# Optimization experiments

Hardware: AMD Instinct MI355X
Metric: run time of the kernel (lower is better)

## Reference

```python
import jax, jax.numpy as jnp
import numpy as np
import math

B, L, D = 2, 2048, 2048
H, DH = 16, 128
R = 16
WIN = 512
EPS = 1e-6


def setup_inputs() -> dict:
    key = jax.random.key(0)
    ks = jax.random.split(key, 16)
    def rn(k, shape, s=1.0):
        return jax.random.normal(k, shape, dtype=jnp.float32) * s
    d_in_std = 1.0 / math.sqrt(D)
    return {
        "x": rn(ks[0], (B, L, D)),
        "norm_w": jnp.ones((D,), jnp.float32),
        "wq": rn(ks[1], (H * DH, D), d_in_std),
        "wk": rn(ks[2], (H * DH, D), d_in_std),
        "wv": rn(ks[3], (H * DH, D), d_in_std),
        "wo": rn(ks[4], (D, H * DH), d_in_std),
        "qA": rn(ks[5], (R, D), 0.02), "qB": rn(ks[6], (H * DH, R), 0.02),
        "kA": rn(ks[7], (R, D), 0.02), "kB": rn(ks[8], (H * DH, R), 0.02),
        "vA": rn(ks[9], (R, D), 0.02), "vB": rn(ks[10], (H * DH, R), 0.02),
        "oA": rn(ks[11], (R, H * DH), 0.02), "oB": rn(ks[12], (D, R), 0.02),
    }


def _lora_proj(h, Wb, A, Bm, scale):
    # y = h @ Wb^T + ((h @ A^T) @ Bm^T) * scale
    return h @ Wb.T + (h @ A.T) @ Bm.T * scale


def _rope_freqs(seq_len, d_head):
    half = d_head // 2
    theta = 1.0 / (10000.0 ** (jnp.arange(half, dtype=jnp.float32) / half))
    freqs = jnp.arange(seq_len, dtype=jnp.float32)[:, None] * theta[None, :]  # (L, half)
    emb = jnp.concatenate([freqs, freqs], axis=-1)  # (L, d_head)
    return jnp.cos(emb), jnp.sin(emb)


def _apply_rope(x, cos, sin):
    # x: (B, H, L, d_head); cos/sin: (L, d_head)
    half = x.shape[-1] // 2
    x1, x2 = x[..., :half], x[..., half:]
    rotated = jnp.concatenate([-x2, x1], axis=-1)
    return x * cos[None, None] + rotated * sin[None, None]


def reference(x, norm_w, wq, wk, wv, wo, qA, qB, kA, kB, vA, vB, oA, oB):
    lora_scale = 1.0 / qA.shape[0]
    residual = x
    # RMSNorm
    h = x * jax.lax.rsqrt(jnp.mean(x * x, axis=-1, keepdims=True) + EPS) * norm_w
    # LoRA-fused projections
    Q = _lora_proj(h, wq, qA, qB, lora_scale)
    K = _lora_proj(h, wk, kA, kB, lora_scale)
    V = _lora_proj(h, wv, vA, vB, lora_scale)
    b, l, _ = x.shape
    Q = Q.reshape(b, l, H, DH).transpose(0, 2, 1, 3)
    K = K.reshape(b, l, H, DH).transpose(0, 2, 1, 3)
    V = V.reshape(b, l, H, DH).transpose(0, 2, 1, 3)
    cos, sin = _rope_freqs(l, DH)
    Q = _apply_rope(Q, cos, sin)
    K = _apply_rope(K, cos, sin)
    # sliding-window causal additive mask (L, L)
    i = jnp.arange(l)[:, None]
    j = jnp.arange(l)[None, :]
    valid = (j <= i) & (j >= i - WIN + 1)
    mask = jnp.where(valid, 0.0, -jnp.inf).astype(x.dtype)
    scores = jnp.einsum("bhqd,bhkd->bhqk", Q, K) / math.sqrt(DH)
    attn = jax.nn.softmax(scores + mask[None, None], axis=-1)
    out = jnp.einsum("bhqk,bhkd->bhqd", attn, V)
    out = out.transpose(0, 2, 1, 3).reshape(b, l, H * DH)
    out = _lora_proj(out, wo, oA, oB, lora_scale)
    return residual + out
```

## Files before the change

### kernel.cpp

```cpp
#include <hip/hip_runtime.h>
#include <hip/hip_bf16.h>

#define LNUM 2048
#define DNUM 2048
#define HNUM 16
#define DHNUM 128
#define MTOK 4096
#define WINSZ 512

typedef __attribute__((ext_vector_type(8))) short bf16x8;
typedef __attribute__((ext_vector_type(4))) short bf16x4;
typedef __attribute__((ext_vector_type(4))) float f32x4;

#define GLOBAL_AS __attribute__((address_space(1)))
#define LDS_AS __attribute__((address_space(3)))
#define BARX asm volatile("s_barrier" ::: "memory")

__device__ __forceinline__ unsigned short f2bf(float f) {
  union { float f; unsigned u; } v; v.f = f;
  unsigned r = v.u + 0x7FFFu + ((v.u >> 16) & 1u);
  return (unsigned short)(r >> 16);
}
__device__ __forceinline__ float bf2f(unsigned short h) {
  union { unsigned u; float f; } v; v.u = ((unsigned)h) << 16;
  return v.f;
}

__global__ __launch_bounds__(256) void weff_k(
    const float* __restrict__ w0, const float* __restrict__ w1,
    const float* __restrict__ w2, const float* __restrict__ w3,
    const float* __restrict__ b0, const float* __restrict__ b1,
    const float* __restrict__ b2, const float* __restrict__ b3,
    const float* __restrict__ a0, const float* __restrict__ a1,
    const float* __restrict__ a2, const float* __restrict__ a3,
    unsigned short* __restrict__ o0, unsigned short* __restrict__ o1,
    unsigned short* __restrict__ o2, unsigned short* __restrict__ o3,
    float s) {
  const int z = blockIdx.z;
  const float* W = z==0?w0:z==1?w1:z==2?w2:w3;
  const float* Bm = z==0?b0:z==1?b1:z==2?b2:b3;
  const float* Am = z==0?a0:z==1?a1:z==2?a2:a3;
  unsigned short* out = z==0?o0:z==1?o1:z==2?o2:o3;

  const int col = blockIdx.x * 1024 + threadIdx.x * 4;
  const int row0 = blockIdx.y * 64;

  float4 av[16];
  #pragma unroll
  for (int j = 0; j < 16; j++) av[j] = *(const float4*)(Am + (size_t)j * DNUM + col);

  for (int r = 0; r < 64; r++) {
    const int n = row0 + r;
    const float* brow = Bm + (size_t)n * 16;
    float dx = 0.f, dy = 0.f, dz = 0.f, dw = 0.f;
    #pragma unroll
    for (int j = 0; j < 16; j++) {
      const float bj = brow[j];
      dx = fmaf(bj, av[j].x, dx); dy = fmaf(bj, av[j].y, dy);
      dz = fmaf(bj, av[j].z, dz); dw = fmaf(bj, av[j].w, dw);
    }
    const float4 wv = *(const float4*)(W + (size_t)n * DNUM + col);
    ushort4 o;
    o.x = f2bf(wv.x + s*dx); o.y = f2bf(wv.y + s*dy);
    o.z = f2bf(wv.z + s*dz); o.w = f2bf(wv.w + s*dw);
    *(ushort4*)(out + (size_t)n * DNUM + col) = o;
  }
}

__global__ __launch_bounds__(256) void rmsnorm_k(const float* __restrict__ x,
                                                 const float* __restrict__ w,
                                                 unsigned short* __restrict__ h) {
  const int row = blockIdx.x;
  const int t = threadIdx.x;
  const float4* xr = (const float4*)(x + (size_t)row * DNUM);
  float4 v0 = xr[t];
  float4 v1 = xr[t + 256];
  float ss = v0.x*v0.x + v0.y*v0.y + v0.z*v0.z + v0.w*v0.w +
             v1.x*v1.x + v1.y*v1.y + v1.z*v1.z + v1.w*v1.w;
  #pragma unroll
  for (int off = 32; off > 0; off >>= 1) ss += __shfl_xor(ss, off);
  __shared__ float red[4];
  if ((t & 63) == 0) red[t >> 6] = ss;
  __syncthreads();
  const float r = rsqrtf((red[0]+red[1]+red[2]+red[3]) * (1.0f/DNUM) + 1e-6f);
  const float4* wr4 = (const float4*)w;
  float4 w0 = wr4[t], w1 = wr4[t+256];
  ushort4 o0, o1;
  o0.x = f2bf(v0.x*r*w0.x); o0.y = f2bf(v0.y*r*w0.y);
  o0.z = f2bf(v0.z*r*w0.z); o0.w = f2bf(v0.w*r*w0.w);
  o1.x = f2bf(v1.x*r*w1.x); o1.y = f2bf(v1.y*r*w1.y);
  o1.z = f2bf(v1.z*r*w1.z); o1.w = f2bf(v1.w*r*w1.w);
  ushort4* hp = (ushort4*)(h + (size_t)row * DNUM);
  hp[t] = o0; hp[t + 256] = o1;
}

__global__ __launch_bounds__(512, 1) void gemmqkv_k(
    const unsigned short* __restrict__ Am,
    const unsigned short* __restrict__ Wall,
    unsigned short* __restrict__ Oall)
{
  const int row0 = blockIdx.y * 256;
  const int col0 = blockIdx.x * 192;
  const int tid = threadIdx.x;
  const int wv = tid >> 6, lane = tid & 63;
  const int wr = wv >> 2, wc = wv & 3;
  const int g = lane >> 4, r4 = lane & 15;

  __shared__ unsigned short lds[57344];

  const int rp = lane >> 2;
  const int sg8 = ((lane & 3) ^ ((rp >> 1) & 3)) * 8;

  auto stage = [&](int buf, int k0) {
    #pragma unroll
    for (int q = 0; q < 4; q++) {
      const int c = q*8 + wv;
      const int kh = c & 1, rc = c >> 1;
      const unsigned short* ga = Am + (size_t)(row0 + rc*16 + rp) * DNUM + k0 + kh*32 + sg8;
      __builtin_amdgcn_global_load_lds((const GLOBAL_AS void*)ga,
          (LDS_AS void*)&lds[buf*16384 + (kh*16 + rc)*512], 16, 0, 0);
    }
    #pragma unroll
    for (int q = 0; q < 3; q++) {
      const int c = q*8 + wv;
      const int kh = c & 1, rc = c >> 1;
      const unsigned short* gb = Wall + (size_t)(col0 + rc*16 + rp) * DNUM + k0 + kh*32 + sg8;
      __builtin_amdgcn_global_load_lds((const GLOBAL_AS void*)gb,
          (LDS_AS void*)&lds[32768 + buf*12288 + (kh*12 + rc)*512], 16, 0, 0);
    }
  };

  f32x4 acc[8][3];
  #pragma unroll
  for (int m = 0; m < 8; m++)
    #pragma unroll
    for (int n = 0; n < 3; n++) acc[m][n] = f32x4{0.f,0.f,0.f,0.f};

  const int cg = (g ^ ((r4 >> 1) & 3)) * 8;

  auto compute = [&](int buf) {
    #pragma unroll
    for (int kh = 0; kh < 2; kh++) {
      const unsigned short* As = &lds[buf*16384 + kh*8192];
      const unsigned short* Bs = &lds[32768 + buf*12288 + kh*6144];
      bf16x8 af[8], bb[3];
      #pragma unroll
      for (int m = 0; m < 8; m++)
        af[m] = *(const bf16x8*)&As[(wr*8 + m)*512 + r4*32 + cg];
      #pragma unroll
      for (int n = 0; n < 3; n++)
        bb[n] = *(const bf16x8*)&Bs[(wc*3 + n)*512 + r4*32 + cg];
      #pragma unroll
      for (int m = 0; m < 8; m++)
        #pragma unroll
        for (int n = 0; n < 3; n++)
          acc[m][n] = __builtin_amdgcn_mfma_f32_16x16x32_bf16(af[m], bb[n], acc[m][n], 0, 0, 0);
    }
  };

  stage(0, 0);
  const int nt = DNUM / 64;
  for (int t = 0; t < nt; t++) {
    if (t < nt - 1) {
      stage((t + 1) & 1, (t + 1) * 64);
      asm volatile("s_waitcnt vmcnt(7)" ::: "memory");
    } else {
      asm volatile("s_waitcnt vmcnt(0)" ::: "memory");
    }
    BARX;
    compute(t & 1);
    BARX;
  }

  #pragma unroll
  for (int m = 0; m < 8; m++) {
    #pragma unroll
    for (int rg = 0; rg < 4; rg++) {
      const int row = row0 + wr*128 + m*16 + 4*g + rg;
      #pragma unroll
      for (int n = 0; n < 3; n++) {
        const int colg = col0 + wc*48 + n*16 + r4;
        const int z = colg >> 11, c = colg & 2047;
        Oall[((size_t)z * MTOK + row) * DNUM + c] = f2bf(acc[m][n][rg]);
      }
    }
  }
}

__global__ __launch_bounds__(512, 1) void gemmo_k(
    const unsigned short* __restrict__ Am,
    const unsigned short* __restrict__ W,
    const float* __restrict__ resid, float* __restrict__ Of)
{
  const int row0 = blockIdx.y * 256;
  const int col0 = blockIdx.x * 128;
  const int tid = threadIdx.x;
  const int wv = tid >> 6, lane = tid & 63;
  const int wr = wv >> 2, wc = wv & 3;
  const int g = lane >> 4, r4 = lane & 15;

  __shared__ unsigned short lds[49152];

  const int rp = lane >> 2;
  const int sg8 = ((lane & 3) ^ ((rp >> 1) & 3)) * 8;

  auto stage = [&](int buf, int k0) {
    #pragma unroll
    for (int q = 0; q < 4; q++) {
      const int c = q*8 + wv;
      const int kh = c & 1, rc = c >> 1;
      const unsigned short* ga = Am + (size_t)(row0 + rc*16 + rp) * DNUM + k0 + kh*32 + sg8;
      __builtin_amdgcn_global_load_lds((const GLOBAL_AS void*)ga,
          (LDS_AS void*)&lds[buf*16384 + (kh*16 + rc)*512], 16, 0, 0);
    }
    #pragma unroll
    for (int q = 0; q < 2; q++) {
      const int c = q*8 + wv;
      const int kh = c & 1, rc = c >> 1;
      const unsigned short* gb = W + (size_t)(col0 + rc*16 + rp) * DNUM + k0 + kh*32 + sg8;
      __builtin_amdgcn_global_load_lds((const GLOBAL_AS void*)gb,
          (LDS_AS void*)&lds[32768 + buf*8192 + (kh*8 + rc)*512], 16, 0, 0);
    }
  };

  f32x4 acc[8][2];
  #pragma unroll
  for (int m = 0; m < 8; m++)
    #pragma unroll
    for (int n = 0; n < 2; n++) acc[m][n] = f32x4{0.f,0.f,0.f,0.f};

  const int cg = (g ^ ((r4 >> 1) & 3)) * 8;

  auto compute = [&](int buf) {
    #pragma unroll
    for (int kh = 0; kh < 2; kh++) {
      const unsigned short* As = &lds[buf*16384 + kh*8192];
      const unsigned short* Bs = &lds[32768 + buf*8192 + kh*4096];
      bf16x8 af[8], bb[2];
      #pragma unroll
      for (int m = 0; m < 8; m++)
        af[m] = *(const bf16x8*)&As[(wr*8 + m)*512 + r4*32 + cg];
      #pragma unroll
      for (int n = 0; n < 2; n++)
        bb[n] = *(const bf16x8*)&Bs[(wc*2 + n)*512 + r4*32 + cg];
      #pragma unroll
      for (int m = 0; m < 8; m++)
        #pragma unroll
        for (int n = 0; n < 2; n++)
          acc[m][n] = __builtin_amdgcn_mfma_f32_16x16x32_bf16(af[m], bb[n], acc[m][n], 0, 0, 0);
    }
  };

  stage(0, 0);
  const int nt = DNUM / 64;
  for (int t = 0; t < nt; t++) {
    if (t < nt - 1) {
      stage((t + 1) & 1, (t + 1) * 64);
      asm volatile("s_waitcnt vmcnt(6)" ::: "memory");
    } else {
      asm volatile("s_waitcnt vmcnt(0)" ::: "memory");
    }
    BARX;
    compute(t & 1);
    BARX;
  }

  #pragma unroll
  for (int m = 0; m < 8; m++) {
    #pragma unroll
    for (int rg = 0; rg < 4; rg++) {
      const int row = row0 + wr*128 + m*16 + 4*g + rg;
      #pragma unroll
      for (int n = 0; n < 2; n++) {
        const int col = col0 + wc*32 + n*16 + r4;
        Of[(size_t)row * DNUM + col] = acc[m][n][rg] + resid[(size_t)row * DNUM + col];
      }
    }
  }
}

__global__ __launch_bounds__(256) void rope_k(unsigned short* __restrict__ Qm,
                                              unsigned short* __restrict__ Km) {
  const int u = blockIdx.x * 256 + threadIdx.x;
  const int t2 = u & 31;
  const int hh = (u >> 5) & (HNUM-1);
  const int i = u >> 9;
  const int l = i & (LNUM - 1);
  const int d0 = 2 * t2;
  const float C = 0.14391156831212787f;
  const float th0 = __expf(-(float)d0 * C);
  const float th1 = __expf(-(float)(d0+1) * C);
  float sn0, cs0, sn1, cs1;
  __sincosf((float)l * th0, &sn0, &cs0);
  __sincosf((float)l * th1, &sn1, &cs1);
  const size_t base = (size_t)i * DNUM + hh * DHNUM + d0;
  const float qs = 0.08838834764831845f;

  unsigned qa = *(const unsigned*)(Qm + base);
  unsigned qb = *(const unsigned*)(Qm + base + 64);
  float a0 = bf2f((unsigned short)qa), a1 = bf2f((unsigned short)(qa >> 16));
  float b0 = bf2f((unsigned short)qb), b1 = bf2f((unsigned short)(qb >> 16));
  unsigned lo = (unsigned)f2bf((a0*cs0 - b0*sn0) * qs) | ((unsigned)f2bf((a1*cs1 - b1*sn1) * qs) << 16);
  unsigned hi = (unsigned)f2bf((b0*cs0 + a0*sn0) * qs) | ((unsigned)f2bf((b1*cs1 + a1*sn1) * qs) << 16);
  *(unsigned*)(Qm + base) = lo;
  *(unsigned*)(Qm + base + 64) = hi;

  unsigned ka = *(const unsigned*)(Km + base);
  unsigned kb = *(const unsigned*)(Km + base + 64);
  a0 = bf2f((unsigned short)ka); a1 = bf2f((unsigned short)(ka >> 16));
  b0 = bf2f((unsigned short)kb); b1 = bf2f((unsigned short)(kb >> 16));
  lo = (unsigned)f2bf(a0*cs0 - b0*sn0) | ((unsigned)f2bf(a1*cs1 - b1*sn1) << 16);
  hi = (unsigned)f2bf(b0*cs0 + a0*sn0) | ((unsigned)f2bf(b1*cs1 + a1*sn1) << 16);
  *(unsigned*)(Km + base) = lo;
  *(unsigned*)(Km + base + 64) = hi;
}

__global__ __launch_bounds__(256) void attn_k(const unsigned short* __restrict__ Q,
                                              const unsigned short* __restrict__ K,
                                              const unsigned short* __restrict__ V,
                                              unsigned short* __restrict__ O) {
  __shared__ unsigned short Kls[8192];
  __shared__ unsigned short Vt[8704];
  const int tid = threadIdx.x, wv = tid >> 6, lane = tid & 63;
  const int g = lane >> 4, r4 = lane & 15;
  const int bidx = blockIdx.x;
  const int q4 = bidx & 31, hh = (bidx >> 5) & 15, b = bidx >> 9;
  const int q_base = q4 * 64;
  const int q0 = q_base + wv * 16;
  const size_t bh = (size_t)b * LNUM * DNUM + (size_t)hh * DHNUM;

  bf16x8 qf[4];
  {
    const unsigned short* qr = Q + bh + (size_t)(q0 + r4) * DNUM;
    #pragma unroll
    for (int dc = 0; dc < 4; dc++) qf[dc] = *(const bf16x8*)(qr + dc*32 + g*8);
  }
  f32x4 oacc[8];
  #pragma unroll
  for (int c = 0; c < 8; c++) oacc[c] = f32x4{0.f,0.f,0.f,0.f};
  float mrun = -1e30f, lrun = 0.f;

  const int qi = q0 + r4;
  const int lo_key = (q_base >= WINSZ) ? (q_base - WINSZ + 1) : 0;
  const int t_lo = lo_key >> 6, t_hi = q_base >> 6;

  const int rp = lane >> 2;
  const int sg = (((lane & 3) ^ ((rp >> 1) & 3))) * 8;
  const int cgr = (g ^ ((r4 >> 1) & 3)) * 8;

  const int vc = wv*8 + (lane >> 3);
  const int vd = lane & 7;

  for (int t64 = t_lo; t64 <= t_hi; t64++) {
    const int k64 = t64 * 64;
    __syncthreads();
    #pragma unroll
    for (int q = 0; q < 4; q++) {
      const unsigned short* src = K + bh + (size_t)(k64 + wv*16 + rp) * DNUM + q*32 + sg;
      __builtin_amdgcn_global_load_lds((const GLOBAL_AS void*)src,
          (LDS_AS void*)&Kls[(q*4 + wv)*512], 16, 0, 0);
    }
    #pragma unroll
    for (int p = 0; p < 2; p++) {
      const int d0 = (vd + 8*p) * 8;
      const unsigned short* vp = V + bh + (size_t)(k64 + 2*vc) * DNUM + d0;
      uint4 va = *(const uint4*)vp;
      uint4 vb = *(const uint4*)(vp + DNUM);
      const unsigned short* as = (const unsigned short*)&va;
      const unsigned short* bs = (const unsigned short*)&vb;
      #pragma unroll
      for (int j = 0; j < 8; j++) {
        *(unsigned*)&Vt[(d0 + j)*68 + 2*vc] = (unsigned)as[j] | ((unsigned)bs[j] << 16);
      }
    }
    __syncthreads();

    #pragma unroll
    for (int kts = 0; kts < 4; kts++) {
      const int k0s = k64 + kts*16;
      if (k0s > q0 + 15 || k0s + 15 < q0 - (WINSZ - 1)) continue;
      f32x4 st = f32x4{0.f,0.f,0.f,0.f};
      #pragma unroll
      for (int dc = 0; dc < 4; dc++) {
        const bf16x8 kf = *(const bf16x8*)&Kls[(dc*4 + kts)*512 + r4*32 + cgr];
        st = __builtin_amdgcn_mfma_f32_16x16x32_bf16(kf, qf[dc], st, 0, 0, 0);
      }
      const int kj = k0s + 4*g;
      const float sv0 = (kj   <= qi && kj   > qi - WINSZ) ? st[0] : -1e30f;
      const float sv1 = (kj+1 <= qi && kj+1 > qi - WINSZ) ? st[1] : -1e30f;
      const float sv2 = (kj+2 <= qi && kj+2 > qi - WINSZ) ? st[2] : -1e30f;
      const float sv3 = (kj+3 <= qi && kj+3 > qi - WINSZ) ? st[3] : -1e30f;
      float pmax = fmaxf(fmaxf(sv0, sv1), fmaxf(sv2, sv3));
      pmax = fmaxf(pmax, __shfl_xor(pmax, 16));
      pmax = fmaxf(pmax, __shfl_xor(pmax, 32));
      const float mnew = fmaxf(mrun, pmax);
      const float sc_old = __expf(mrun - mnew);
      const float p0 = __expf(sv0 - mnew), p1 = __expf(sv1 - mnew);
      const float p2 = __expf(sv2 - mnew), p3 = __expf(sv3 - mnew);
      float psum = p0 + p1 + p2 + p3;
      psum += __shfl_xor(psum, 16);
      psum += __shfl_xor(psum, 32);
      lrun = lrun * sc_old + psum;
      mrun = mnew;
      bf16x4 pf;
      pf[0] = (short)f2bf(p0); pf[1] = (short)f2bf(p1);
      pf[2] = (short)f2bf(p2); pf[3] = (short)f2bf(p3);
      #pragma unroll
      for (int c = 0; c < 8; c++) {
        oacc[c][0] *= sc_old; oacc[c][1] *= sc_old;
        oacc[c][2] *= sc_old; oacc[c][3] *= sc_old;
      }
      #pragma unroll
      for (int dblk = 0; dblk < 8; dblk++) {
        const bf16x4 vf = *(const bf16x4*)&Vt[(dblk*16 + r4)*68 + kts*16 + 4*g];
        oacc[dblk] = __builtin_amdgcn_mfma_f32_16x16x16bf16_1k(vf, pf, oacc[dblk], 0, 0, 0);
      }
    }
  }

  __syncthreads();
  unsigned short* scr = &Vt[wv * 2176];
  const float inv = 1.0f / lrun;
  #pragma unroll
  for (int dblk = 0; dblk < 8; dblk++) {
    #pragma unroll
    for (int rg = 0; rg < 4; rg++) {
      scr[r4*136 + dblk*16 + 4*g + rg] = f2bf(oacc[dblk][rg] * inv);
    }
  }
  #pragma unroll
  for (int p = 0; p < 4; p++) {
    const int qq = p*4 + g;
    const uint4 vvv = *(const uint4*)(scr + qq*136 + r4*8);
    *(uint4*)(O + bh + (size_t)(q0 + qq) * DNUM + r4*8) = vvv;
  }
}

extern "C" void kernel_launch(void* const* d_in, const int* in_sizes, int n_in,
                              void* d_out, int out_size, void* d_ws, size_t ws_size,
                              hipStream_t stream) {
  (void)in_sizes; (void)n_in; (void)out_size; (void)ws_size;
  const float* x     = (const float*)d_in[0];
  const float* normw = (const float*)d_in[1];
  const float* wq = (const float*)d_in[2];
  const float* wk = (const float*)d_in[3];
  const float* wvm = (const float*)d_in[4];
  const float* wo = (const float*)d_in[5];
  const float* qA = (const float*)d_in[6];
  const float* qB = (const float*)d_in[7];
  const float* kA = (const float*)d_in[8];
  const float* kB = (const float*)d_in[9];
  const float* vA = (const float*)d_in[10];
  const float* vB = (const float*)d_in[11];
  const float* oA = (const float*)d_in[12];
  const float* oB = (const float*)d_in[13];

  char* w = (char*)d_ws;
  const size_t SZ = (size_t)MTOK * DNUM * 2;
  unsigned short* h  = (unsigned short*)(w);
  unsigned short* Qb = (unsigned short*)(w + SZ);
  unsigned short* Kb = (unsigned short*)(w + 2*SZ);
  unsigned short* Vb = (unsigned short*)(w + 3*SZ);
  unsigned short* AO = (unsigned short*)(w + 4*SZ);
  unsigned short* Wq = (unsigned short*)(w + 5*SZ);
  unsigned short* Wk = Wq + (size_t)DNUM*DNUM;
  unsigned short* Wv = Wk + (size_t)DNUM*DNUM;
  unsigned short* Wo = Wv + (size_t)DNUM*DNUM;

  const float lscale = 1.0f / 16.0f;

  weff_k<<<dim3(2, 32, 4), 256, 0, stream>>>(wq, wk, wvm, wo,
                                             qB, kB, vB, oB,
                                             qA, kA, vA, oA,
                                             Wq, Wk, Wv, Wo, lscale);
  rmsnorm_k<<<dim3(4096), 256, 0, stream>>>(x, normw, h);
  gemmqkv_k<<<dim3(32, 16), 512, 0, stream>>>(h, Wq, Qb);
  rope_k<<<dim3(8192), 256, 0, stream>>>(Qb, Kb);
  attn_k<<<dim3(1024), 256, 0, stream>>>(Qb, Kb, Vb, AO);
  gemmo_k<<<dim3(16, 16), 512, 0, stream>>>(AO, Wo, x, (float*)d_out);
}
```

Measured before the change: 260.2 us.

## Enlarge attention tiles to 128 queries, add lazy softmax rescale and interior-mask fast path

The attention kernel now runs 8 waves per block over 128 queries, so each K/V tile loaded into LDS is shared by twice as many query rows. K and V loading is split across the 8 waves. Masking is skipped for interior tiles that lie fully inside the window. The online softmax only rescales the accumulators when the running max grows by more than a threshold, which removes most exp and multiply work but lets unnormalized values grow up to about e^8. The weight-merge kernel also uses more blocks with fewer rows each to raise parallelism.

```diff
diff --git a/kernel.cpp b/kernel.cpp
--- a/kernel.cpp
+++ b/kernel.cpp
@@ -43,13 +43,13 @@
   unsigned short* out = z==0?o0:z==1?o1:z==2?o2:o3;
 
   const int col = blockIdx.x * 1024 + threadIdx.x * 4;
-  const int row0 = blockIdx.y * 64;
+  const int row0 = blockIdx.y * 16;
 
   float4 av[16];
   #pragma unroll
   for (int j = 0; j < 16; j++) av[j] = *(const float4*)(Am + (size_t)j * DNUM + col);
 
-  for (int r = 0; r < 64; r++) {
+  for (int r = 0; r < 16; r++) {
     const int n = row0 + r;
     const float* brow = Bm + (size_t)n * 16;
     float dx = 0.f, dy = 0.f, dz = 0.f, dw = 0.f;
@@ -315,17 +315,18 @@
   *(unsigned*)(Km + base + 64) = hi;
 }
 
-__global__ __launch_bounds__(256) void attn_k(const unsigned short* __restrict__ Q,
+__global__ __launch_bounds__(512) void attn_k(const unsigned short* __restrict__ Q,
                                               const unsigned short* __restrict__ K,
                                               const unsigned short* __restrict__ V,
                                               unsigned short* __restrict__ O) {
-  __shared__ unsigned short Kls[8192];
-  __shared__ unsigned short Vt[8704];
+  __shared__ unsigned short shm[17408];
+  unsigned short* Kls = shm;
+  unsigned short* Vt  = shm + 8192;
   const int tid = threadIdx.x, wv = tid >> 6, lane = tid & 63;
   const int g = lane >> 4, r4 = lane & 15;
   const int bidx = blockIdx.x;
-  const int q4 = bidx & 31, hh = (bidx >> 5) & 15, b = bidx >> 9;
-  const int q_base = q4 * 64;
+  const int q7 = bidx & 15, hh = (bidx >> 4) & 15, b = bidx >> 8;
+  const int q_base = q7 * 128;
   const int q0 = q_base + wv * 16;
   const size_t bh = (size_t)b * LNUM * DNUM + (size_t)hh * DHNUM;
 
@@ -341,28 +342,29 @@
   float mrun = -1e30f, lrun = 0.f;
 
   const int qi = q0 + r4;
-  const int lo_key = (q_base >= WINSZ) ? (q_base - WINSZ + 1) : 0;
-  const int t_lo = lo_key >> 6, t_hi = q_base >> 6;
+  const int t_lo = (q_base >= WINSZ) ? ((q_base - WINSZ + 1) >> 6) : 0;
+  const int t_hi = (q_base + 127) >> 6;
 
   const int rp = lane >> 2;
   const int sg = (((lane & 3) ^ ((rp >> 1) & 3))) * 8;
   const int cgr = (g ^ ((r4 >> 1) & 3)) * 8;
 
-  const int vc = wv*8 + (lane >> 3);
-  const int vd = lane & 7;
+  const int vc = tid & 31;
+  const int vd = tid >> 5;
 
   for (int t64 = t_lo; t64 <= t_hi; t64++) {
     const int k64 = t64 * 64;
     __syncthreads();
     #pragma unroll
-    for (int q = 0; q < 4; q++) {
-      const unsigned short* src = K + bh + (size_t)(k64 + wv*16 + rp) * DNUM + q*32 + sg;
+    for (int qq = 0; qq < 2; qq++) {
+      const int c = wv*2 + qq;
+      const int dc = c >> 2, kc = c & 3;
+      const unsigned short* src = K + bh + (size_t)(k64 + kc*16 + rp) * DNUM + dc*32 + sg;
       __builtin_amdgcn_global_load_lds((const GLOBAL_AS void*)src,
-          (LDS_AS void*)&Kls[(q*4 + wv)*512], 16, 0, 0);
-    }
-    #pragma unroll
-    for (int p = 0; p < 2; p++) {
-      const int d0 = (vd + 8*p) * 8;
+          (LDS_AS void*)&Kls[(dc*4 + kc)*512], 16, 0, 0);
+    }
+    {
+      const int d0 = vd * 8;
       const unsigned short* vp = V + bh + (size_t)(k64 + 2*vc) * DNUM + d0;
       uint4 va = *(const uint4*)vp;
       uint4 vb = *(const uint4*)(vp + DNUM);
@@ -385,32 +387,44 @@
         const bf16x8 kf = *(const bf16x8*)&Kls[(dc*4 + kts)*512 + r4*32 + cgr];
         st = __builtin_amdgcn_mfma_f32_16x16x32_bf16(kf, qf[dc], st, 0, 0, 0);
       }
-      const int kj = k0s + 4*g;
-      const float sv0 = (kj   <= qi && kj   > qi - WINSZ) ? st[0] : -1e30f;
-      const float sv1 = (kj+1 <= qi && kj+1 > qi - WINSZ) ? st[1] : -1e30f;
-      const float sv2 = (kj+2 <= qi && kj+2 > qi - WINSZ) ? st[2] : -1e30f;
-      const float sv3 = (kj+3 <= qi && kj+3 > qi - WINSZ) ? st[3] : -1e30f;
+      float sv0, sv1, sv2, sv3;
+      const bool interior = (k0s + 15 <= q0) && (k0s >= q0 - (WINSZ - 16));
+      if (interior) {
+        sv0 = st[0]; sv1 = st[1]; sv2 = st[2]; sv3 = st[3];
+      } else {
+        const int kj = k0s + 4*g;
+        sv0 = (kj   <= qi && kj   > qi - WINSZ) ? st[0] : -INFINITY;
+        sv1 = (kj+1 <= qi && kj+1 > qi - WINSZ) ? st[1] : -INFINITY;
+        sv2 = (kj+2 <= qi && kj+2 > qi - WINSZ) ? st[2] : -INFINITY;
+        sv3 = (kj+3 <= qi && kj+3 > qi - WINSZ) ? st[3] : -INFINITY;
+      }
       float pmax = fmaxf(fmaxf(sv0, sv1), fmaxf(sv2, sv3));
       pmax = fmaxf(pmax, __shfl_xor(pmax, 16));
       pmax = fmaxf(pmax, __shfl_xor(pmax, 32));
-      const float mnew = fmaxf(mrun, pmax);
-      const float sc_old = __expf(mrun - mnew);
+      float mnew;
+      if (__all(pmax - mrun <= 8.0f)) {
+        mnew = mrun;
+      } else {
+        mnew = fmaxf(mrun, pmax);
+        const float sc = __expf(mrun - mnew);
+        lrun *= sc;
+        #pragma unroll
+        for (int c = 0; c < 8; c++) {
+          oacc[c][0] *= sc; oacc[c][1] *= sc;
+          oacc[c][2] *= sc; oacc[c][3] *= sc;
+        }
+        mrun = mnew;
+      }
       const float p0 = __expf(sv0 - mnew), p1 = __expf(sv1 - mnew);
       const float p2 = __expf(sv2 - mnew), p3 = __expf(sv3 - mnew);
       float psum = p0 + p1 + p2 + p3;
       psum += __shfl_xor(psum, 16);
       psum += __shfl_xor(psum, 32);
-      lrun = lrun * sc_old + psum;
-      mrun = mnew;
+      lrun += psum;
       bf16x4 pf;
       pf[0] = (short)f2bf(p0); pf[1] = (short)f2bf(p1);
       pf[2] = (short)f2bf(p2); pf[3] = (short)f2bf(p3);
       #pragma unroll
-      for (int c = 0; c < 8; c++) {
-        oacc[c][0] *= sc_old; oacc[c][1] *= sc_old;
-        oacc[c][2] *= sc_old; oacc[c][3] *= sc_old;
-      }
-      #pragma unroll
       for (int dblk = 0; dblk < 8; dblk++) {
         const bf16x4 vf = *(const bf16x4*)&Vt[(dblk*16 + r4)*68 + kts*16 + 4*g];
         oacc[dblk] = __builtin_amdgcn_mfma_f32_16x16x16bf16_1k(vf, pf, oacc[dblk], 0, 0, 0);
@@ -419,7 +433,7 @@
   }
 
   __syncthreads();
-  unsigned short* scr = &Vt[wv * 2176];
+  unsigned short* scr = &shm[wv * 2176];
   const float inv = 1.0f / lrun;
   #pragma unroll
   for (int dblk = 0; dblk < 8; dblk++) {
@@ -469,13 +483,13 @@
 
   const float lscale = 1.0f / 16.0f;
 
-  weff_k<<<dim3(2, 32, 4), 256, 0, stream>>>(wq, wk, wvm, wo,
-                                             qB, kB, vB, oB,
-                                             qA, kA, vA, oA,
-                                             Wq, Wk, Wv, Wo, lscale);
+  weff_k<<<dim3(2, 128, 4), 256, 0, stream>>>(wq, wk, wvm, wo,
+                                              qB, kB, vB, oB,
+                                              qA, kA, vA, oA,
+                                              Wq, Wk, Wv, Wo, lscale);
   rmsnorm_k<<<dim3(4096), 256, 0, stream>>>(x, normw, h);
   gemmqkv_k<<<dim3(32, 16), 512, 0, stream>>>(h, Wq, Qb);
   rope_k<<<dim3(8192), 256, 0, stream>>>(Qb, Kb);
-  attn_k<<<dim3(1024), 256, 0, stream>>>(Qb, Kb, Vb, AO);
+  attn_k<<<dim3(512), 512, 0, stream>>>(Qb, Kb, Vb, AO);
   gemmo_k<<<dim3(16, 16), 512, 0, stream>>>(AO, Wo, x, (float*)d_out);
 }
```

Result: faster. 223.3 us (-14.2%).
